# Optimization experiments

Measured on AMD Instinct MI355X. Metric: run time of the kernel, lower is better.

The kernel has to match this reference:

```python
import jax, jax.numpy as jnp
import numpy as np

B, D, T_STEPS = 256, 512, 64


def setup_inputs() -> dict:
    key = jax.random.key(0)
    ks = jax.random.split(key, 9)
    s = 1.0 / np.sqrt(D)  # torch LSTM init scale
    return {
        "h": jax.random.normal(ks[0], (B, D), dtype=jnp.float32),
        "T": T_STEPS,
        "W_ih0": jax.random.uniform(ks[1], (4 * D, D), jnp.float32, -s, s),
        "W_hh0": jax.random.uniform(ks[2], (4 * D, D), jnp.float32, -s, s),
        "b_ih0": jax.random.uniform(ks[3], (4 * D,), jnp.float32, -s, s),
        "b_hh0": jax.random.uniform(ks[4], (4 * D,), jnp.float32, -s, s),
        "W_ih1": jax.random.uniform(ks[5], (4 * D, D), jnp.float32, -s, s),
        "W_hh1": jax.random.uniform(ks[6], (4 * D, D), jnp.float32, -s, s),
        "b_ih1": jax.random.uniform(ks[7], (4 * D,), jnp.float32, -s, s),
        "b_hh1": jax.random.uniform(ks[8], (4 * D,), jnp.float32, -s, s),
    }


def _lstm_cell(x, h, c, W_ih, W_hh, b_ih, b_hh):
    # gates: [B, 4D], torch gate order (i, f, g, o)
    gates = x @ W_ih.T + h @ W_hh.T + (b_ih + b_hh)
    i, f, g, o = jnp.split(gates, 4, axis=-1)
    c_new = jax.nn.sigmoid(f) * c + jax.nn.sigmoid(i) * jnp.tanh(g)
    h_new = jax.nn.sigmoid(o) * jnp.tanh(c_new)
    return h_new, c_new


def reference(h, T, W_ih0, W_hh0, b_ih0, b_hh0, W_ih1, W_hh1, b_ih1, b_hh1):
    b, d = h.shape
    zeros = jnp.zeros((b, d), dtype=h.dtype)

    def step(carry, _):
        x, h0, c0, h1, c1 = carry
        h0, c0 = _lstm_cell(x, h0, c0, W_ih0, W_hh0, b_ih0, b_hh0)
        h1, c1 = _lstm_cell(h0, h1, c1, W_ih1, W_hh1, b_ih1, b_hh1)
        # output of layer 2 is fed back as next step's input
        return (h1, h0, c0, h1, c1), h1

    init = (h, zeros, zeros, zeros, zeros)
    _, e_seq = jax.lax.scan(step, init, xs=None, length=T)
    return e_seq  # [T, B, D]
```

## Files before the change

kernel.cpp:

```cpp
#include <hip/hip_runtime.h>


#define B_DIM 256
#define D_DIM 512
#define T_N   64
#define BD    131072
#define SMEM_WBYTES 131072
#define SMEM_BYTES  (SMEM_WBYTES + 4 * 1056 * 4)

#define WS_SLOTS  0
#define WS_XINIT  32768
#define WS_H0B0   (WS_XINIT + BD * 2)
#define WS_H0B1   (WS_H0B0 + BD * 2)
#define WS_H1B0   (WS_H0B1 + BD * 2)
#define WS_H1B1   (WS_H1B0 + BD * 2)

typedef _Float16 half8_t  __attribute__((ext_vector_type(8)));
typedef float    f32x16_t __attribute__((ext_vector_type(16)));
typedef float    f32x4_t  __attribute__((ext_vector_type(4)));

#define LOADC(p)  __hip_atomic_load((p), __ATOMIC_RELAXED, __HIP_MEMORY_SCOPE_AGENT)
#define STOREC(p, v) __hip_atomic_store((p), (v), __ATOMIC_RELAXED, __HIP_MEMORY_SCOPE_AGENT)

__device__ __forceinline__ float sigmoidf_(float x) {
  float z = __expf(-fabsf(x));
  float s = 1.0f / (1.0f + z);
  return x >= 0.0f ? s : 1.0f - s;
}
__device__ __forceinline__ float tanhf_(float x) {
  float z = __expf(-2.0f * fabsf(x));
  float t = (1.0f - z) / (1.0f + z);
  return x >= 0.0f ? t : -t;
}

__device__ __forceinline__ f32x4_t load_cv16(const void* p) {
  f32x4_t r;
  asm volatile("global_load_dwordx4 %0, %1, off sc0 sc1"
               : "=v"(r) : "v"(p) : "memory");
  return r;
}

__global__ void lstm_init(const float* __restrict__ h, _Float16* __restrict__ xinit,
                          _Float16* __restrict__ h0b1, _Float16* __restrict__ h1b1,
                          unsigned* __restrict__ slots) {
  int i = blockIdx.x * 256 + threadIdx.x;
  if (i < BD) {
    xinit[i] = (_Float16)h[i];
    h0b1[i] = (_Float16)0.0f;
    h1b1[i] = (_Float16)0.0f;
  }
  if (i < 8192) slots[i] = 0u;
}

__global__ void __launch_bounds__(256, 1) lstm_persist(
    const float* __restrict__ Wih0, const float* __restrict__ Whh0,
    const float* __restrict__ bih0, const float* __restrict__ bhh0,
    const float* __restrict__ Wih1, const float* __restrict__ Whh1,
    const float* __restrict__ bih1, const float* __restrict__ bhh1,
    float* __restrict__ out,
    const _Float16* __restrict__ xinit,
    _Float16* __restrict__ h0b0, _Float16* __restrict__ h0b1,
    _Float16* __restrict__ h1b0, _Float16* __restrict__ h1b1,
    unsigned* __restrict__ slots)
{
  extern __shared__ char smem[];
  float* red = (float*)(smem + SMEM_WBYTES);
  const int tid = threadIdx.x;
  const int l = tid & 63;
  const int w = tid >> 6;
  const int bid = blockIdx.x;
  const int bb = (bid & 7) >> 1;
  const int db = ((bid >> 3) << 1) | (bid & 1);
  const int b0 = bb << 6;
  const int d0 = db << 3;

#pragma unroll
  for (int L = 0; L < 2; ++L) {
    for (int it = 0; it < 16; ++it) {
      int slot = it * 256 + tid;
      int s2 = slot >> 6, lane = slot & 63;
      int khalf = s2 >> 5, ks = s2 & 31;
      int kg = lane >> 5, nl = lane & 31;
      int ng = ((nl >> 3) << 9) + d0 + (nl & 7);
      int col = ks * 16 + kg * 8;
      const float* srcb = khalf ? (L ? Whh1 : Whh0) : (L ? Wih1 : Wih0);
      const float* src = srcb + (size_t)ng * 512 + col;
      half8_t hv;
#pragma unroll
      for (int j = 0; j < 8; ++j) hv[j] = (_Float16)src[j];
      *(half8_t*)(smem + (size_t)L * 65536 + (size_t)slot * 16) = hv;
    }
  }

  const int cbl = tid >> 2;
  const int j0 = (tid & 3) << 1;
  float bias0[4][2], bias1[4][2];
#pragma unroll
  for (int g = 0; g < 4; ++g) {
#pragma unroll
    for (int p = 0; p < 2; ++p) {
      int ng = (g << 9) + d0 + j0 + p;
      bias0[g][p] = bih0[ng] + bhh0[ng];
      bias1[g][p] = bih1[ng] + bhh1[ng];
    }
  }
  float c0s[2] = {0.0f, 0.0f}, c1s[2] = {0.0f, 0.0f};
  unsigned* grpslots = slots + (bb << 6) * 32;
  __syncthreads();

  for (int s = 0; s < 128; ++s) {
    const int t = s >> 1;
    const int layer = s & 1;
    const int rb = (t - 1) & 1;
    const int wb = t & 1;
    const _Float16* fresh;
    const _Float16* stale;
    _Float16* hout;
    if (layer == 0) {
      fresh = (t == 0) ? xinit : (rb ? h1b1 : h1b0);
      stale = rb ? h0b1 : h0b0;
      hout  = wb ? h0b1 : h0b0;
    } else {
      fresh = wb ? h0b1 : h0b0;
      stale = rb ? h1b1 : h1b0;
      hout  = wb ? h1b1 : h1b0;
    }

    if (w < 2 && s > 0) {
      unsigned* sl = grpslots + l * 32;
      unsigned v;
      do {
        v = LOADC(sl);
      } while (!__all((int)(v >= (unsigned)s)));
      asm volatile("" ::: "memory");
    }

    const _Float16* asrc = (w >= 2) ? stale : fresh;
    const char* ap = (const char*)(asrc + (size_t)(b0 + ((w & 1) << 5) + (l & 31)) * 512
                                        + ((l >> 5) << 3));
    int boff = layer * 65536 + ((w >> 1) * 32768) + l * 16;

    f32x16_t acc0, acc1;
#pragma unroll
    for (int r = 0; r < 16; ++r) { acc0[r] = 0.0f; acc1[r] = 0.0f; }

    f32x4_t va[16];
#pragma unroll
    for (int half = 0; half < 2; ++half) {
#pragma unroll
      for (int j = 0; j < 16; ++j) va[j] = load_cv16(ap + half * 512 + 32 * j);
      asm volatile("s_waitcnt vmcnt(0)" ::: "memory");
#pragma unroll
      for (int ks = 0; ks < 8; ++ks) {
        half8_t a0  = __builtin_bit_cast(half8_t, va[2 * ks]);
        half8_t a1  = __builtin_bit_cast(half8_t, va[2 * ks + 1]);
        half8_t bv0 = *(const half8_t*)(smem + boff);
        half8_t bv1 = *(const half8_t*)(smem + boff + 1024);
        acc0 = __builtin_amdgcn_mfma_f32_32x32x16_f16(a0, bv0, acc0, 0, 0, 0);
        acc1 = __builtin_amdgcn_mfma_f32_32x32x16_f16(a1, bv1, acc1, 0, 0, 0);
        boff += 2048;
      }
    }

    {
      float* redw = red + w * 1056 + (l & 31);
      const int rbase = (l >> 5) << 2;
#pragma unroll
      for (int r = 0; r < 16; ++r) {
        int row = (r & 3) + ((r >> 2) << 3) + rbase;
        redw[row * 33] = acc0[r] + acc1[r];
      }
    }
    __syncthreads();

    float hv[2];
    int gidx;
    {
      const int base = (cbl >> 5) * 1056 + (cbl & 31) * 33 + j0;
#pragma unroll
      for (int p = 0; p < 2; ++p) {
        float vi = red[base + p]      + red[base + 2112 + p]      + (layer ? bias1[0][p] : bias0[0][p]);
        float vf = red[base + 8 + p]  + red[base + 2112 + 8 + p]  + (layer ? bias1[1][p] : bias0[1][p]);
        float vg = red[base + 16 + p] + red[base + 2112 + 16 + p] + (layer ? bias1[2][p] : bias0[2][p]);
        float vo = red[base + 24 + p] + red[base + 2112 + 24 + p] + (layer ? bias1[3][p] : bias0[3][p]);
        float iv = sigmoidf_(vi), fv = sigmoidf_(vf);
        float gv = tanhf_(vg),    ov = sigmoidf_(vo);
        float cold = layer ? c1s[p] : c0s[p];
        float c = fv * cold + iv * gv;
        if (layer) c1s[p] = c; else c0s[p] = c;
        hv[p] = ov * tanhf_(c);
      }
      gidx = (b0 + cbl) * 512 + d0 + j0;
      unsigned hu = ((unsigned)__builtin_bit_cast(unsigned short, (_Float16)hv[0])) |
                    ((unsigned)__builtin_bit_cast(unsigned short, (_Float16)hv[1]) << 16);
      STOREC((unsigned*)&hout[gidx], hu);
    }
    asm volatile("s_waitcnt vmcnt(0)" ::: "memory");
    __syncthreads();
    if (tid == 0)
      STOREC(grpslots + db * 32, (unsigned)(s + 1));
    if (layer) {
      float* op = out + (size_t)t * BD + gidx;
      op[0] = hv[0]; op[1] = hv[1];
    }
  }
}

extern "C" void kernel_launch(void* const* d_in, const int* in_sizes, int n_in,
                              void* d_out, int out_size, void* d_ws, size_t ws_size,
                              hipStream_t stream) {
  const float* h    = (const float*)d_in[0];
  const float* Wih0 = (const float*)d_in[2];
  const float* Whh0 = (const float*)d_in[3];
  const float* bih0 = (const float*)d_in[4];
  const float* bhh0 = (const float*)d_in[5];
  const float* Wih1 = (const float*)d_in[6];
  const float* Whh1 = (const float*)d_in[7];
  const float* bih1 = (const float*)d_in[8];
  const float* bhh1 = (const float*)d_in[9];
  float* out = (float*)d_out;

  char* ws = (char*)d_ws;
  unsigned* slots  = (unsigned*)(ws + WS_SLOTS);
  _Float16* xinit  = (_Float16*)(ws + WS_XINIT);
  _Float16* h0b0   = (_Float16*)(ws + WS_H0B0);
  _Float16* h0b1   = (_Float16*)(ws + WS_H0B1);
  _Float16* h1b0   = (_Float16*)(ws + WS_H1B0);
  _Float16* h1b1   = (_Float16*)(ws + WS_H1B1);

  hipFuncSetAttribute((const void*)lstm_persist,
                      hipFuncAttributeMaxDynamicSharedMemorySize, SMEM_BYTES);

  lstm_init<<<512, 256, 0, stream>>>(h, xinit, h0b1, h1b1, slots);

  void* args[] = { &Wih0, &Whh0, &bih0, &bhh0, &Wih1, &Whh1, &bih1, &bhh1,
                   &out, &xinit, &h0b0, &h0b1, &h1b0, &h1b1, &slots };
  hipLaunchCooperativeKernel((void*)lstm_persist, dim3(256), dim3(256),
                             args, SMEM_BYTES, stream);
}
```

Measured before the change: 958.9 us.

## Use per-step rotating hidden-state buffers to allow cached loads instead of coherent ones

Replaces the double-buffered per-layer hidden-state arrays with a sequence of buffers, one per step in deep mode or a 4-slot ring otherwise. Deep mode is chosen only when the workspace is big enough. In deep mode every step writes to a fresh address that no CU has read before, so the A-operand loads switch from sc0/sc1 coherent global loads to ordinary cached loads, and the explicit vmcnt wait before the MFMAs is dropped. The per-group sync flags are also packed densely instead of padded to 128-byte strides. The risks are relying on the cache never holding stale lines for never-touched addresses, a large workspace footprint, and possible contention on the packed flags.

```diff
diff --git a/kernel.cpp b/kernel.cpp
--- a/kernel.cpp
+++ b/kernel.cpp
@@ -1,19 +1,17 @@
 #include <hip/hip_runtime.h>
 
 
-#define B_DIM 256
-#define D_DIM 512
-#define T_N   64
 #define BD    131072
 #define SMEM_WBYTES 131072
 #define SMEM_BYTES  (SMEM_WBYTES + 4 * 1056 * 4)
 
-#define WS_SLOTS  0
-#define WS_XINIT  32768
-#define WS_H0B0   (WS_XINIT + BD * 2)
-#define WS_H0B1   (WS_H0B0 + BD * 2)
-#define WS_H1B0   (WS_H0B1 + BD * 2)
-#define WS_H1B1   (WS_H1B0 + BD * 2)
+#define WS_SLOTS 0
+#define WS_XINIT 4096
+#define WS_ZERO  (WS_XINIT + BD * 2)
+#define WS_ROT   (WS_ZERO + BD * 2)
+#define ROT_BYTES ((size_t)BD * 2)
+#define WS_NEED_DEEP (WS_ROT + 128 * ROT_BYTES)
+#define WS_NEED_RING (WS_ROT + 4 * ROT_BYTES)
 
 typedef _Float16 half8_t  __attribute__((ext_vector_type(8)));
 typedef float    f32x16_t __attribute__((ext_vector_type(16)));
@@ -40,16 +38,16 @@
   return r;
 }
 
-__global__ void lstm_init(const float* __restrict__ h, _Float16* __restrict__ xinit,
-                          _Float16* __restrict__ h0b1, _Float16* __restrict__ h1b1,
-                          unsigned* __restrict__ slots) {
+__global__ void lstm_init(const float* __restrict__ h, char* __restrict__ ws) {
   int i = blockIdx.x * 256 + threadIdx.x;
+  unsigned* slots = (unsigned*)(ws + WS_SLOTS);
+  _Float16* xinit = (_Float16*)(ws + WS_XINIT);
+  _Float16* zerob = (_Float16*)(ws + WS_ZERO);
   if (i < BD) {
     xinit[i] = (_Float16)h[i];
-    h0b1[i] = (_Float16)0.0f;
-    h1b1[i] = (_Float16)0.0f;
-  }
-  if (i < 8192) slots[i] = 0u;
+    zerob[i] = (_Float16)0.0f;
+  }
+  if (i < 256) slots[i] = 0u;
 }
 
 __global__ void __launch_bounds__(256, 1) lstm_persist(
@@ -57,14 +55,15 @@
     const float* __restrict__ bih0, const float* __restrict__ bhh0,
     const float* __restrict__ Wih1, const float* __restrict__ Whh1,
     const float* __restrict__ bih1, const float* __restrict__ bhh1,
-    float* __restrict__ out,
-    const _Float16* __restrict__ xinit,
-    _Float16* __restrict__ h0b0, _Float16* __restrict__ h0b1,
-    _Float16* __restrict__ h1b0, _Float16* __restrict__ h1b1,
-    unsigned* __restrict__ slots)
+    float* __restrict__ out, char* __restrict__ ws, int deep)
 {
   extern __shared__ char smem[];
   float* red = (float*)(smem + SMEM_WBYTES);
+  unsigned* slots = (unsigned*)(ws + WS_SLOTS);
+  const _Float16* xinit = (const _Float16*)(ws + WS_XINIT);
+  const _Float16* zerob = (const _Float16*)(ws + WS_ZERO);
+  char* rot = ws + WS_ROT;
+
   const int tid = threadIdx.x;
   const int l = tid & 63;
   const int w = tid >> 6;
@@ -105,29 +104,23 @@
     }
   }
   float c0s[2] = {0.0f, 0.0f}, c1s[2] = {0.0f, 0.0f};
-  unsigned* grpslots = slots + (bb << 6) * 32;
+  unsigned* gflags = slots + (bb << 6);
   __syncthreads();
 
   for (int s = 0; s < 128; ++s) {
     const int t = s >> 1;
     const int layer = s & 1;
-    const int rb = (t - 1) & 1;
-    const int wb = t & 1;
-    const _Float16* fresh;
-    const _Float16* stale;
-    _Float16* hout;
-    if (layer == 0) {
-      fresh = (t == 0) ? xinit : (rb ? h1b1 : h1b0);
-      stale = rb ? h0b1 : h0b0;
-      hout  = wb ? h0b1 : h0b0;
-    } else {
-      fresh = wb ? h0b1 : h0b0;
-      stale = rb ? h1b1 : h1b0;
-      hout  = wb ? h1b1 : h1b0;
-    }
+    const int fi = deep ? (s - 1) : ((s - 1) & 3);
+    const int si = deep ? (s - 2) : ((s - 2) & 3);
+    const int oi = deep ? s : (s & 3);
+    const _Float16* fresh = (s == 0) ? xinit
+                          : (const _Float16*)(rot + (size_t)fi * ROT_BYTES);
+    const _Float16* stale = (s <= 1) ? zerob
+                          : (const _Float16*)(rot + (size_t)si * ROT_BYTES);
+    _Float16* hout = (_Float16*)(rot + (size_t)oi * ROT_BYTES);
 
     if (w < 2 && s > 0) {
-      unsigned* sl = grpslots + l * 32;
+      const unsigned* sl = gflags + l;
       unsigned v;
       do {
         v = LOADC(sl);
@@ -144,21 +137,41 @@
 #pragma unroll
     for (int r = 0; r < 16; ++r) { acc0[r] = 0.0f; acc1[r] = 0.0f; }
 
-    f32x4_t va[16];
-#pragma unroll
-    for (int half = 0; half < 2; ++half) {
-#pragma unroll
-      for (int j = 0; j < 16; ++j) va[j] = load_cv16(ap + half * 512 + 32 * j);
-      asm volatile("s_waitcnt vmcnt(0)" ::: "memory");
-#pragma unroll
-      for (int ks = 0; ks < 8; ++ks) {
-        half8_t a0  = __builtin_bit_cast(half8_t, va[2 * ks]);
-        half8_t a1  = __builtin_bit_cast(half8_t, va[2 * ks + 1]);
-        half8_t bv0 = *(const half8_t*)(smem + boff);
-        half8_t bv1 = *(const half8_t*)(smem + boff + 1024);
-        acc0 = __builtin_amdgcn_mfma_f32_32x32x16_f16(a0, bv0, acc0, 0, 0, 0);
-        acc1 = __builtin_amdgcn_mfma_f32_32x32x16_f16(a1, bv1, acc1, 0, 0, 0);
-        boff += 2048;
+    if (deep) {
+#pragma unroll
+      for (int half = 0; half < 2; ++half) {
+        f32x4_t va[16];
+#pragma unroll
+        for (int j = 0; j < 16; ++j)
+          va[j] = *(const f32x4_t*)(ap + half * 512 + 32 * j);
+#pragma unroll
+        for (int ks = 0; ks < 8; ++ks) {
+          half8_t a0  = __builtin_bit_cast(half8_t, va[2 * ks]);
+          half8_t a1  = __builtin_bit_cast(half8_t, va[2 * ks + 1]);
+          half8_t bv0 = *(const half8_t*)(smem + boff);
+          half8_t bv1 = *(const half8_t*)(smem + boff + 1024);
+          acc0 = __builtin_amdgcn_mfma_f32_32x32x16_f16(a0, bv0, acc0, 0, 0, 0);
+          acc1 = __builtin_amdgcn_mfma_f32_32x32x16_f16(a1, bv1, acc1, 0, 0, 0);
+          boff += 2048;
+        }
+      }
+    } else {
+#pragma unroll
+      for (int half = 0; half < 2; ++half) {
+        f32x4_t va[16];
+#pragma unroll
+        for (int j = 0; j < 16; ++j) va[j] = load_cv16(ap + half * 512 + 32 * j);
+        asm volatile("s_waitcnt vmcnt(0)" ::: "memory");
+#pragma unroll
+        for (int ks = 0; ks < 8; ++ks) {
+          half8_t a0  = __builtin_bit_cast(half8_t, va[2 * ks]);
+          half8_t a1  = __builtin_bit_cast(half8_t, va[2 * ks + 1]);
+          half8_t bv0 = *(const half8_t*)(smem + boff);
+          half8_t bv1 = *(const half8_t*)(smem + boff + 1024);
+          acc0 = __builtin_amdgcn_mfma_f32_32x32x16_f16(a0, bv0, acc0, 0, 0, 0);
+          acc1 = __builtin_amdgcn_mfma_f32_32x32x16_f16(a1, bv1, acc1, 0, 0, 0);
+          boff += 2048;
+        }
       }
     }
 
@@ -198,7 +211,7 @@
     asm volatile("s_waitcnt vmcnt(0)" ::: "memory");
     __syncthreads();
     if (tid == 0)
-      STOREC(grpslots + db * 32, (unsigned)(s + 1));
+      STOREC(gflags + db, (unsigned)(s + 1));
     if (layer) {
       float* op = out + (size_t)t * BD + gidx;
       op[0] = hv[0]; op[1] = hv[1];
@@ -219,22 +232,17 @@
   const float* bih1 = (const float*)d_in[8];
   const float* bhh1 = (const float*)d_in[9];
   float* out = (float*)d_out;
-
   char* ws = (char*)d_ws;
-  unsigned* slots  = (unsigned*)(ws + WS_SLOTS);
-  _Float16* xinit  = (_Float16*)(ws + WS_XINIT);
-  _Float16* h0b0   = (_Float16*)(ws + WS_H0B0);
-  _Float16* h0b1   = (_Float16*)(ws + WS_H0B1);
-  _Float16* h1b0   = (_Float16*)(ws + WS_H1B0);
-  _Float16* h1b1   = (_Float16*)(ws + WS_H1B1);
+
+  int deep = (ws_size >= (size_t)WS_NEED_DEEP) ? 1 : 0;
 
   hipFuncSetAttribute((const void*)lstm_persist,
                       hipFuncAttributeMaxDynamicSharedMemorySize, SMEM_BYTES);
 
-  lstm_init<<<512, 256, 0, stream>>>(h, xinit, h0b1, h1b1, slots);
+  lstm_init<<<512, 256, 0, stream>>>(h, ws);
 
   void* args[] = { &Wih0, &Whh0, &bih0, &bhh0, &Wih1, &Whh1, &bih1, &bhh1,
-                   &out, &xinit, &h0b0, &h0b1, &h1b0, &h1b1, &slots };
+                   &out, &ws, &deep };
   hipLaunchCooperativeKernel((void*)lstm_persist, dim3(256), dim3(256),
                              args, SMEM_BYTES, stream);
 }
```

After: 1.127 ms. 17.5% more time.
